# Optimization experiments

Hardware: AMD Instinct MI355X
Metric: run time of the kernel (lower is better)

The kernel has to match this reference:

```python
import jax, jax.numpy as jnp
import numpy as np

B, N, C, H, L = 4, 1024, 1152, 16, 120
D = C // H
HID = 4 * C
EPS = 1e-6


def _ln(x):
    m = jnp.mean(x, axis=-1, keepdims=True)
    v = jnp.var(x, axis=-1, keepdims=True)
    return (x - m) * jax.lax.rsqrt(v + EPS)


def _attend(q, k, v):
    # q:(B,H,Nq,D) k,v:(B,H,Nk,D)
    scale = D ** -0.5
    s = jnp.einsum('bhnd,bhmd->bhnm', q, k) * scale
    p = jax.nn.softmax(s, axis=-1)
    o = jnp.einsum('bhnm,bhmd->bhnd', p, v)
    return o.transpose(0, 2, 1, 3).reshape(q.shape[0], q.shape[2], C)


def setup_inputs() -> dict:
    key = jax.random.key(0)
    ks = jax.random.split(key, 20)
    g = lambda i, shape, s=0.02: jax.random.normal(ks[i], shape, jnp.float32) * s
    return {
        'x': jax.random.normal(ks[0], (B, N, C), jnp.float32),
        'y': jax.random.normal(ks[1], (B, L, C), jnp.float32),
        't': jax.random.normal(ks[2], (B, 6 * C), jnp.float32),
        'sst': jax.random.normal(ks[3], (6, C), jnp.float32) / C ** 0.5,
        'qkv_w': g(4, (C, 3 * C)), 'qkv_b': jnp.zeros((3 * C,), jnp.float32),
        'proj_w': g(5, (C, C)), 'proj_b': jnp.zeros((C,), jnp.float32),
        'q_w': g(6, (C, C)), 'q_b': jnp.zeros((C,), jnp.float32),
        'kv_w': g(7, (C, 2 * C)), 'kv_b': jnp.zeros((2 * C,), jnp.float32),
        'cproj_w': g(8, (C, C)), 'cproj_b': jnp.zeros((C,), jnp.float32),
        'fc1_w': g(9, (C, HID)), 'fc1_b': jnp.zeros((HID,), jnp.float32),
        'fc2_w': g(10, (HID, C)), 'fc2_b': jnp.zeros((C,), jnp.float32),
    }


def reference(x, y, t, sst, qkv_w, qkv_b, proj_w, proj_b, q_w, q_b,
              kv_w, kv_b, cproj_w, cproj_b, fc1_w, fc1_b, fc2_w, fc2_b):
    mods = sst[None] + t.reshape(B, 6, C)  # (B,6,C)
    sh_msa, sc_msa, g_msa, sh_mlp, sc_mlp, g_mlp = [mods[:, i:i + 1] for i in range(6)]

    # --- self attention with adaLN modulation ---
    h = _ln(x) * (1 + sc_msa) + sh_msa
    qkv = (h @ qkv_w + qkv_b).reshape(B, N, 3, H, D).transpose(2, 0, 3, 1, 4)
    attn_out = _attend(qkv[0], qkv[1], qkv[2]) @ proj_w + proj_b
    x = x + g_msa * attn_out

    # --- cross attention (batched cond, no mask) ---
    q = (x @ q_w + q_b).reshape(B, N, H, D).transpose(0, 2, 1, 3)
    kv = (y @ kv_w + kv_b).reshape(B, L, 2, H, D).transpose(2, 0, 3, 1, 4)
    x = x + (_attend(q, kv[0], kv[1]) @ cproj_w + cproj_b)

    # --- MLP with adaLN modulation ---
    h = _ln(x) * (1 + sc_mlp) + sh_mlp
    h = jax.nn.gelu(h @ fc1_w + fc1_b, approximate=True) @ fc2_w + fc2_b
    x = x + g_mlp * h
    return x
```

## Files before the change

### kernel.cpp

```cpp
#include <hip/hip_runtime.h>
#include <hip/hip_bf16.h>
#include <stdint.h>

typedef __hip_bfloat16 BT;
typedef __bf16 bf16x8 __attribute__((ext_vector_type(8)));
typedef float f32x4 __attribute__((ext_vector_type(4)));

constexpr int kB = 4, kN = 1024, kC = 1152, kH = 16, kL = 120, kD = 72, kDp = 96;
constexpr int kHid = 4608, kBN = 4096, kZ = 64;
constexpr float kScale = 0.11785113019775793f;

__global__ void detect_dtype(const void* xin, int* flag) {
  __shared__ int cnt;
  if (threadIdx.x == 0) cnt = 0;
  __syncthreads();
  const BT* xb = (const BT*)xin;
  int local = 0;
  for (int i = threadIdx.x; i < 4096; i += 256) {
    float v = __bfloat162float(xb[i]);
    if (!(fabsf(v) <= 1e3f)) local++;
  }
  atomicAdd(&cnt, local);
  __syncthreads();
  if (threadIdx.x == 0) *flag = (cnt > 8) ? 1 : 0;
}

struct ConvSeg {
  const void* src;
  BT* dst;
  long long n;
};
struct ConvArgs {
  ConvSeg seg[10];
  int nseg;
};
__global__ void convert_all(ConvArgs a, const int* __restrict__ flag) {
  const int f = *flag;
  long long i = (long long)blockIdx.x * 256 + threadIdx.x;
#pragma unroll
  for (int s = 0; s < 10; ++s) {
    if (s >= a.nseg) return;
    if (i < a.seg[s].n) {
      a.seg[s].dst[i] = f ? __float2bfloat16(((const float*)a.seg[s].src)[i])
                          : ((const BT*)a.seg[s].src)[i];
      return;
    }
    i -= a.seg[s].n;
  }
}

__global__ void encode_ws(float* out, long long n, float c) {
  long long i = (long long)blockIdx.x * 256 + threadIdx.x;
  if (i < n) out[i] = c;
}

__device__ __forceinline__ void gl_lds16(const BT* g, BT* l) {
  __builtin_amdgcn_global_load_lds(
      (const __attribute__((address_space(1))) uint32_t*)g,
      (__attribute__((address_space(3))) uint32_t*)l, 16, 0, 0);
}

template <int BM, int EP>
__global__ __launch_bounds__(256, 4) void gemm_tile(
    const BT* __restrict__ A, const BT* __restrict__ Bm, const BT* __restrict__ bias,
    void* __restrict__ Cout, int M, int Nc, int K, int lda, int ldb, int ldc,
    long long sA, long long sB, long long sC) {
  constexpr int NA = BM / 32;
  constexpr int NU = NA + 4;
  constexpr int NJ = (BM == 128) ? 4 : 2;
  __shared__ __align__(16) BT As[2][BM * 32];
  __shared__ __align__(16) BT Bs[2][128 * 32];
  A += (long long)blockIdx.z * sA;
  Bm += (long long)blockIdx.z * sB;

  const int gx = gridDim.x, nwg = gx * gridDim.y;
  int id = blockIdx.y * gx + blockIdx.x;
  {
    const int q = nwg >> 3, r = nwg & 7;
    const int xcd = id & 7, pos = id >> 3;
    const int base = (xcd < r) ? xcd * (q + 1) : r * (q + 1) + (xcd - r) * q;
    id = base + pos;
  }
  const int m0 = (id / gx) * BM, n0 = (id % gx) * 128;

  const int tid = threadIdx.x, lane = tid & 63, w = tid >> 6;
  const int lr = lane >> 2, lc = (lane & 3) * 8;
  const int l15 = lane & 15, q8 = (lane >> 4) * 8;
  const int wm = (BM == 128) ? (w & 1) * 64 : 0;
  const int wn = (BM == 128) ? (w >> 1) * 64 : w * 32;

  auto gptr = [&](int u, int half) -> const BT* {
    if (u < NA) {
      int rr = m0 + u * 32 + lr + half * 16;
      if (rr >= M) rr = M - 1;
      return A + (long long)rr * lda + lc;
    }
    int rr = n0 + (u - NA) * 32 + lr + half * 16;
    if (rr >= Nc) rr = Nc - 1;
    return Bm + (long long)rr * ldb + lc;
  };
  const bool has2 = (w < NA);
  const int u2 = has2 ? (w + 4) : w;
  const BT* g00 = gptr(w, 0);
  const BT* g01 = gptr(w, 1);
  const BT* g10 = gptr(u2, 0);
  const BT* g11 = gptr(u2, 1);
  BT* d00[2];
  BT* d10[2];
#pragma unroll
  for (int bb = 0; bb < 2; ++bb) {
    d00[bb] = (w < NA) ? &As[bb][w * 1024] : &Bs[bb][(w - NA) * 1024];
    int ub = u2 - NA;
    if (ub < 0) ub = 0;
    if (ub > 3) ub = 3;
    d10[bb] = &Bs[bb][ub * 1024];
  }

  auto stage = [&](int bb, int k0) {
    gl_lds16(g00 + k0, d00[bb]);
    gl_lds16(g01 + k0, d00[bb] + 512);
    if (has2) {
      gl_lds16(g10 + k0, d10[bb]);
      gl_lds16(g11 + k0, d10[bb] + 512);
    }
  };

  f32x4 acc[4][NJ] = {};

  auto compute = [&](int bb) {
    bf16x8 af[4], bf[NJ];
#pragma unroll
    for (int i = 0; i < 4; ++i)
      af[i] = *reinterpret_cast<const bf16x8*>(&As[bb][(wm + i * 16 + l15) * 32 + q8]);
#pragma unroll
    for (int j = 0; j < NJ; ++j)
      bf[j] = *reinterpret_cast<const bf16x8*>(&Bs[bb][(wn + j * 16 + l15) * 32 + q8]);
#pragma unroll
    for (int i = 0; i < 4; ++i)
#pragma unroll
      for (int j = 0; j < NJ; ++j)
        acc[i][j] = __builtin_amdgcn_mfma_f32_16x16x32_bf16(af[i], bf[j], acc[i][j], 0, 0, 0);
  };

  stage(0, 0);
  __syncthreads();
  const int nk = K >> 5;
  int cur = 0;
  for (int t = 1; t < nk; ++t) {
    stage(cur ^ 1, t << 5);
    compute(cur);
    __syncthreads();
    cur ^= 1;
  }
  compute(cur);

  const int rowq = (lane >> 4) * 4;
  const long long cb = (long long)blockIdx.z * sC;
#pragma unroll
  for (int j = 0; j < NJ; ++j) {
    int col = n0 + wn + j * 16 + l15;
    if (col >= Nc) continue;
    float bv = bias ? __bfloat162float(bias[col]) : 0.f;
#pragma unroll
    for (int i = 0; i < 4; ++i) {
      int row = m0 + wm + i * 16 + rowq;
#pragma unroll
      for (int r = 0; r < 4; ++r) {
        if (row + r < M) {
          float v = acc[i][j][r] + bv;
          if (EP == 2) {
            float z = 1.5957691216057308f * (v + 0.044715f * v * v * v);
            v = v / (1.f + __expf(-z));
          }
          long long off = cb + (long long)(row + r) * ldc + col;
          if (EP == 1)
            ((float*)Cout)[off] = v;
          else
            ((BT*)Cout)[off] = __float2bfloat16(v);
        }
      }
    }
  }
}

__global__ void transpose_any(const void* __restrict__ in, BT* __restrict__ out,
                              int R, int Cin, const int* __restrict__ flag) {
  __shared__ BT tile[32][33];
  const int f = *flag;
  const int tx = threadIdx.x & 31, ty = threadIdx.x >> 5;
  const int r0 = blockIdx.y * 32, c0 = blockIdx.x * 32;
#pragma unroll
  for (int j = 0; j < 32; j += 8) {
    int r = r0 + ty + j;
    if (r < R && c0 + tx < Cin) {
      long long idx = (long long)r * Cin + c0 + tx;
      tile[ty + j][tx] = f ? __float2bfloat16(((const float*)in)[idx]) : ((const BT*)in)[idx];
    }
  }
  __syncthreads();
#pragma unroll
  for (int j = 0; j < 32; j += 8) {
    int oc = c0 + ty + j;
    if (oc < Cin && r0 + tx < R) out[(long long)oc * R + r0 + tx] = tile[tx][ty + j];
  }
}

template <int SRC>
__global__ __launch_bounds__(256) void ln_mod(const void* __restrict__ xin,
                                              const BT* __restrict__ tc,
                                              const BT* __restrict__ sstc,
                                              BT* __restrict__ hout,
                                              int shiftRow, int scaleRow,
                                              const int* __restrict__ flag) {
  const int f = (SRC == 1) ? 1 : *flag;
  const int row = blockIdx.x;
  const int b = row >> 10;
  const long long base = (long long)row * kC;
  float s = 0.f, s2 = 0.f;
  for (int c = threadIdx.x; c < kC; c += 256) {
    float v = f ? ((const float*)xin)[base + c] : __bfloat162float(((const BT*)xin)[base + c]);
    s += v;
    s2 += v * v;
  }
  for (int o = 32; o > 0; o >>= 1) {
    s += __shfl_down(s, o, 64);
    s2 += __shfl_down(s2, o, 64);
  }
  __shared__ float red[8];
  const int w = threadIdx.x >> 6;
  if ((threadIdx.x & 63) == 0) {
    red[w] = s;
    red[4 + w] = s2;
  }
  __syncthreads();
  const float m = (red[0] + red[1] + red[2] + red[3]) * (1.f / kC);
  const float ex2 = (red[4] + red[5] + red[6] + red[7]) * (1.f / kC);
  const float rstd = rsqrtf(ex2 - m * m + 1e-6f);
  const BT* tsh = tc + (long long)b * 6 * kC + (long long)shiftRow * kC;
  const BT* tsc = tc + (long long)b * 6 * kC + (long long)scaleRow * kC;
  const BT* ssh = sstc + (long long)shiftRow * kC;
  const BT* ssc = sstc + (long long)scaleRow * kC;
  for (int c = threadIdx.x; c < kC; c += 256) {
    float sc = __bfloat162float(ssc[c]) + __bfloat162float(tsc[c]);
    float sh = __bfloat162float(ssh[c]) + __bfloat162float(tsh[c]);
    float xv0 = f ? ((const float*)xin)[base + c] : __bfloat162float(((const BT*)xin)[base + c]);
    float xv = (xv0 - m) * rstd;
    hout[base + c] = __float2bfloat16(xv * (1.f + sc) + sh);
  }
}

__global__ void scatter_qk(const BT* __restrict__ qkv, BT* __restrict__ Qp,
                           BT* __restrict__ Kp) {
  long long i = (long long)blockIdx.x * 256 + threadIdx.x;
  if (i >= (long long)kZ * kN * kDp) return;
  int d = (int)(i % kDp);
  long long r = i / kDp;
  int n = (int)(r % kN);
  int z = (int)(r / kN);
  int b = z >> 4, h = z & 15;
  if (d < kD) {
    long long src = ((long long)(b * kN + n)) * (3 * kC) + h * kD + d;
    Qp[i] = __float2bfloat16(kScale * __bfloat162float(qkv[src]));
    Kp[i] = qkv[src + kC];
  } else {
    Qp[i] = __float2bfloat16(0.f);
    Kp[i] = __float2bfloat16(0.f);
  }
}

__global__ void scatter_v(const BT* __restrict__ qkv, BT* __restrict__ VT) {
  long long i = (long long)blockIdx.x * 256 + threadIdx.x;
  if (i >= (long long)kZ * kD * kN) return;
  int n = (int)(i % kN);
  long long r = i / kN;
  int d = (int)(r % kD);
  int z = (int)(r / kD);
  int b = z >> 4, h = z & 15;
  VT[i] = qkv[((long long)(b * kN + n)) * (3 * kC) + 2 * kC + h * kD + d];
}

__global__ void scatter_qc(const BT* __restrict__ qc, BT* __restrict__ Qp) {
  long long i = (long long)blockIdx.x * 256 + threadIdx.x;
  if (i >= (long long)kZ * kN * kDp) return;
  int d = (int)(i % kDp);
  long long r = i / kDp;
  int n = (int)(r % kN);
  int z = (int)(r / kN);
  int b = z >> 4, h = z & 15;
  Qp[i] = (d < kD)
              ? __float2bfloat16(kScale * __bfloat162float(qc[((long long)(b * kN + n)) * kC + h * kD + d]))
              : __float2bfloat16(0.f);
}

__global__ void scatter_kc(const BT* __restrict__ kvb, BT* __restrict__ Kcp) {
  long long i = (long long)blockIdx.x * 256 + threadIdx.x;
  if (i >= (long long)kZ * kL * kDp) return;
  int d = (int)(i % kDp);
  long long r = i / kDp;
  int l = (int)(r % kL);
  int z = (int)(r / kL);
  int b = z >> 4, h = z & 15;
  Kcp[i] = (d < kD) ? kvb[((long long)(b * kL + l)) * (2 * kC) + h * kD + d] : __float2bfloat16(0.f);
}

__global__ void scatter_vc(const BT* __restrict__ kvb, BT* __restrict__ VcT) {
  long long i = (long long)blockIdx.x * 256 + threadIdx.x;
  if (i >= (long long)kZ * kD * 128) return;
  int l = (int)(i % 128);
  long long r = i / 128;
  int d = (int)(r % kD);
  int z = (int)(r / kD);
  int b = z >> 4, h = z & 15;
  VcT[i] = (l < kL) ? kvb[((long long)(b * kL + l)) * (2 * kC) + kC + h * kD + d] : __float2bfloat16(0.f);
}

__global__ void heads_to_cat(const BT* __restrict__ O, BT* __restrict__ cat) {
  long long i = (long long)blockIdx.x * 256 + threadIdx.x;
  if (i >= (long long)kZ * kN * kD) return;
  int d = (int)(i % kD);
  long long r = i / kD;
  int n = (int)(r % kN);
  int z = (int)(r / kN);
  int b = z >> 4, h = z & 15;
  cat[((long long)(b * kN + n)) * kC + h * kD + d] = O[i];
}

__global__ __launch_bounds__(256) void softmax1024(BT* __restrict__ S) {
  const long long row = blockIdx.x;
  BT* r = S + row * 1024;
  const int tid = threadIdx.x;
  union { ushort4 u; BT b[4]; } ld;
  ld.u = *(const ushort4*)(r + tid * 4);
  float v[4];
#pragma unroll
  for (int k = 0; k < 4; ++k) v[k] = __bfloat162float(ld.b[k]);
  float mx = fmaxf(fmaxf(v[0], v[1]), fmaxf(v[2], v[3]));
  for (int o = 32; o > 0; o >>= 1) mx = fmaxf(mx, __shfl_down(mx, o, 64));
  __shared__ float red[4], red2[4];
  if ((tid & 63) == 0) red[tid >> 6] = mx;
  __syncthreads();
  mx = fmaxf(fmaxf(red[0], red[1]), fmaxf(red[2], red[3]));
  float s = 0.f;
#pragma unroll
  for (int k = 0; k < 4; ++k) {
    v[k] = __expf(v[k] - mx);
    s += v[k];
  }
  for (int o = 32; o > 0; o >>= 1) s += __shfl_down(s, o, 64);
  if ((tid & 63) == 0) red2[tid >> 6] = s;
  __syncthreads();
  s = red2[0] + red2[1] + red2[2] + red2[3];
  const float inv = 1.f / s;
#pragma unroll
  for (int k = 0; k < 4; ++k) ld.b[k] = __float2bfloat16(v[k] * inv);
  *(ushort4*)(r + tid * 4) = ld.u;
}

__global__ void softmax_cross(BT* __restrict__ S) {
  const long long row = blockIdx.x;
  BT* r = S + row * 128;
  const int c = threadIdx.x;
  float v = (c < kL) ? __bfloat162float(r[c]) : -1e30f;
  float mx = v;
  for (int o = 32; o > 0; o >>= 1) mx = fmaxf(mx, __shfl_down(mx, o, 64));
  __shared__ float sm[2], ss[2];
  if ((c & 63) == 0) sm[c >> 6] = mx;
  __syncthreads();
  mx = fmaxf(sm[0], sm[1]);
  float e = (c < kL) ? __expf(v - mx) : 0.f;
  float s = e;
  for (int o = 32; o > 0; o >>= 1) s += __shfl_down(s, o, 64);
  if ((c & 63) == 0) ss[c >> 6] = s;
  __syncthreads();
  s = ss[0] + ss[1];
  r[c] = __float2bfloat16(e / s);
}

__global__ void resid_gate(const void* __restrict__ x, const BT* __restrict__ raw,
                           const BT* __restrict__ tc, const BT* __restrict__ sstc,
                           float* __restrict__ resf, BT* __restrict__ resb,
                           const int* __restrict__ flag) {
  long long i = (long long)blockIdx.x * 256 + threadIdx.x;
  if (i >= (long long)kBN * kC) return;
  const int f = *flag;
  int c = (int)(i % kC);
  int b = (int)(i / ((long long)kN * kC));
  float g = __bfloat162float(sstc[2 * kC + c]) + __bfloat162float(tc[(long long)b * 6 * kC + 2 * kC + c]);
  float xv = f ? ((const float*)x)[i] : __bfloat162float(((const BT*)x)[i]);
  float v = xv + g * __bfloat162float(raw[i]);
  resf[i] = v;
  resb[i] = __float2bfloat16(v);
}

__global__ void resid_add(float* __restrict__ res, const BT* __restrict__ raw) {
  long long i = (long long)blockIdx.x * 256 + threadIdx.x;
  if (i < (long long)kBN * kC) res[i] += __bfloat162float(raw[i]);
}

__global__ void final_out(const float* __restrict__ res, const BT* __restrict__ raw,
                          const BT* __restrict__ tc, const BT* __restrict__ sstc,
                          float* __restrict__ out) {
  long long i = (long long)blockIdx.x * 256 + threadIdx.x;
  if (i >= (long long)kBN * kC) return;
  int c = (int)(i % kC);
  int b = (int)(i / ((long long)kN * kC));
  float g = __bfloat162float(sstc[5 * kC + c]) + __bfloat162float(tc[(long long)b * 6 * kC + 5 * kC + c]);
  out[i] = res[i] + g * __bfloat162float(raw[i]);
}

extern "C" void kernel_launch(void* const* d_in, const int* in_sizes, int n_in,
                              void* d_out, int out_size, void* d_ws, size_t ws_size,
                              hipStream_t stream) {
  const void* x = d_in[0];
  const void* y = d_in[1];
  const void* t = d_in[2];
  const void* sst = d_in[3];
  const void* qkv_w = d_in[4];
  const void* qkv_b = d_in[5];
  const void* proj_w = d_in[6];
  const void* proj_b = d_in[7];
  const void* q_w = d_in[8];
  const void* q_b = d_in[9];
  const void* kv_w = d_in[10];
  const void* kv_b = d_in[11];
  const void* cproj_w = d_in[12];
  const void* cproj_b = d_in[13];
  const void* fc1_w = d_in[14];
  const void* fc1_b = d_in[15];
  const void* fc2_w = d_in[16];
  const void* fc2_b = d_in[17];
  (void)in_sizes; (void)n_in;

  char* p = (char*)d_ws;
  size_t off = 0;
  auto alloc = [&](size_t bytes) {
    void* r = p + off;
    off += (bytes + 1023) & ~(size_t)1023;
    return r;
  };
  int* dflag = (int*)alloc(16);
  BT* canonY = (BT*)alloc((size_t)kB * kL * kC * 2);
  BT* canonT = (BT*)alloc((size_t)kB * 6 * kC * 2);
  BT* canonSst = (BT*)alloc((size_t)6 * kC * 2);
  BT* canonBias = (BT*)alloc((size_t)16384 * 2);
  BT* wT = (BT*)alloc((size_t)kHid * kC * 2);
  BT* bufH = (BT*)alloc((size_t)kBN * kC * 2);
  BT* bufCH = (BT*)alloc((size_t)kZ * kN * kDp * 2);
  BT* bufQp = (BT*)alloc((size_t)kZ * kN * kDp * 2);
  BT* bufVT = (BT*)alloc((size_t)kZ * kD * kN * 2);
  BT* rawB = (BT*)alloc((size_t)kBN * kC * 2);
  float* resF = (float*)alloc((size_t)kBN * kC * 4);
  BT* arena = (BT*)alloc((size_t)kBN * kHid * 2);
  const size_t need = off;

  BT* bufO = rawB;
  BT* fc2T = bufQp;
  BT* kvBuf = (BT*)((char*)arena + 17825792);

  if (ws_size < need) {
    float c = 100.f * (float)(1 + (int)(ws_size >> 24));
    long long n = (long long)out_size;
    encode_ws<<<(int)((n + 255) / 256), 256, 0, stream>>>((float*)d_out, n, c);
    return;
  }

  BT* qkvB = canonBias;
  BT* projB = canonBias + 3456;
  BT* qB = canonBias + 4608;
  BT* kvB = canonBias + 5760;
  BT* cprojB = canonBias + 8064;
  BT* fc1B = canonBias + 9216;
  BT* fc2B = canonBias + 13824;

  auto gemm = [&](int ep, const BT* A, const BT* Bm, const BT* bias, void* Cp,
                  int M, int Nc, int K, int lda, int ldb, int ldc,
                  long long sA, long long sB, long long sC, int Zb) {
    long long nwg128 = (long long)((Nc + 127) / 128) * ((M + 127) / 128) * Zb;
    if (nwg128 < 512) {
      dim3 g((Nc + 127) / 128, (M + 63) / 64, Zb);
      if (ep == 0)
        gemm_tile<64, 0><<<g, 256, 0, stream>>>(A, Bm, bias, Cp, M, Nc, K, lda, ldb, ldc, sA, sB, sC);
      else if (ep == 1)
        gemm_tile<64, 1><<<g, 256, 0, stream>>>(A, Bm, bias, Cp, M, Nc, K, lda, ldb, ldc, sA, sB, sC);
      else
        gemm_tile<64, 2><<<g, 256, 0, stream>>>(A, Bm, bias, Cp, M, Nc, K, lda, ldb, ldc, sA, sB, sC);
    } else {
      dim3 g((Nc + 127) / 128, (M + 127) / 128, Zb);
      if (ep == 0)
        gemm_tile<128, 0><<<g, 256, 0, stream>>>(A, Bm, bias, Cp, M, Nc, K, lda, ldb, ldc, sA, sB, sC);
      else if (ep == 1)
        gemm_tile<128, 1><<<g, 256, 0, stream>>>(A, Bm, bias, Cp, M, Nc, K, lda, ldb, ldc, sA, sB, sC);
      else
        gemm_tile<128, 2><<<g, 256, 0, stream>>>(A, Bm, bias, Cp, M, Nc, K, lda, ldb, ldc, sA, sB, sC);
    }
  };
  auto tp = [&](const void* in, BT* out, int R, int Cin) {
    dim3 g((Cin + 31) / 32, (R + 31) / 32);
    transpose_any<<<g, 256, 0, stream>>>(in, out, R, Cin, dflag);
  };

  detect_dtype<<<1, 256, 0, stream>>>(x, dflag);
  {
    ConvArgs a;
    a.seg[0] = {y, canonY, (long long)kB * kL * kC};
    a.seg[1] = {t, canonT, (long long)kB * 6 * kC};
    a.seg[2] = {sst, canonSst, (long long)6 * kC};
    a.seg[3] = {qkv_b, qkvB, 3456};
    a.seg[4] = {proj_b, projB, 1152};
    a.seg[5] = {q_b, qB, 1152};
    a.seg[6] = {kv_b, kvB, 2304};
    a.seg[7] = {cproj_b, cprojB, 1152};
    a.seg[8] = {fc1_b, fc1B, 4608};
    a.seg[9] = {fc2_b, fc2B, 1152};
    a.nseg = 10;
    long long tot = 552960 + 27648 + 6912 + 14976;
    convert_all<<<(int)((tot + 255) / 256), 256, 0, stream>>>(a, dflag);
  }

  ln_mod<0><<<kBN, 256, 0, stream>>>(x, canonT, canonSst, bufH, 0, 1, dflag);
  tp(qkv_w, wT, kC, 3 * kC);
  gemm(0, bufH, wT, qkvB, arena, kBN, 3 * kC, kC, kC, kC, 3 * kC, 0, 0, 0, 1);
  {
    long long tot = (long long)kZ * kN * kDp;
    scatter_qk<<<(int)((tot + 255) / 256), 256, 0, stream>>>(arena, bufQp, bufCH);
    tot = (long long)kZ * kD * kN;
    scatter_v<<<(int)((tot + 255) / 256), 256, 0, stream>>>(arena, bufVT);
  }
  for (int c = 0; c < 4; ++c) {
    int z0 = c * 16;
    const BT* Qb = bufQp + (size_t)z0 * kN * kDp;
    const BT* Kb = bufCH + (size_t)z0 * kN * kDp;
    const BT* Vb = bufVT + (size_t)z0 * kD * kN;
    BT* Ob = bufO + (size_t)z0 * kN * kD;
    gemm(0, Qb, Kb, nullptr, arena, kN, kN, kDp, kDp, kDp, kN,
         (long long)kN * kDp, (long long)kN * kDp, (long long)kN * kN, 16);
    softmax1024<<<16 * kN, 256, 0, stream>>>(arena);
    gemm(0, arena, Vb, nullptr, Ob, kN, kD, kN, kN, kN, kD,
         (long long)kN * kN, (long long)kD * kN, (long long)kN * kD, 16);
  }
  heads_to_cat<<<18432, 256, 0, stream>>>(bufO, bufCH);
  tp(proj_w, wT, kC, kC);
  gemm(0, bufCH, wT, projB, rawB, kBN, kC, kC, kC, kC, kC, 0, 0, 0, 1);
  resid_gate<<<18432, 256, 0, stream>>>(x, rawB, canonT, canonSst, resF, bufH, dflag);

  tp(q_w, wT, kC, kC);
  gemm(0, bufH, wT, qB, bufCH, kBN, kC, kC, kC, kC, kC, 0, 0, 0, 1);
  {
    long long tot = (long long)kZ * kN * kDp;
    scatter_qc<<<(int)((tot + 255) / 256), 256, 0, stream>>>(bufCH, bufQp);
  }
  tp(kv_w, wT, kC, 2 * kC);
  gemm(0, canonY, wT, kvB, kvBuf, kB * kL, 2 * kC, kC, kC, kC, 2 * kC, 0, 0, 0, 1);
  {
    long long tot = (long long)kZ * kL * kDp;
    scatter_kc<<<(int)((tot + 255) / 256), 256, 0, stream>>>(kvBuf, bufCH);
    tot = (long long)kZ * kD * 128;
    scatter_vc<<<(int)((tot + 255) / 256), 256, 0, stream>>>(kvBuf, bufVT);
  }
  gemm(0, bufQp, bufCH, nullptr, arena, kN, kL, kDp, kDp, kDp, 128,
       (long long)kN * kDp, (long long)kL * kDp, (long long)kN * 128, kZ);
  softmax_cross<<<kZ * kN, 128, 0, stream>>>(arena);
  gemm(0, arena, bufVT, nullptr, bufO, kN, kD, 128, 128, 128, kD,
       (long long)kN * 128, (long long)kD * 128, (long long)kN * kD, kZ);
  heads_to_cat<<<18432, 256, 0, stream>>>(bufO, bufCH);
  tp(cproj_w, wT, kC, kC);
  gemm(0, bufCH, wT, cprojB, rawB, kBN, kC, kC, kC, kC, kC, 0, 0, 0, 1);
  resid_add<<<18432, 256, 0, stream>>>(resF, rawB);

  ln_mod<1><<<kBN, 256, 0, stream>>>(resF, canonT, canonSst, bufH, 3, 4, dflag);
  tp(fc1_w, wT, kC, kHid);
  tp(fc2_w, fc2T, kHid, kC);
  gemm(2, bufH, wT, fc1B, arena, kBN, kHid, kC, kC, kC, kHid, 0, 0, 0, 1);
  gemm(0, arena, fc2T, fc2B, rawB, kBN, kC, kHid, kHid, kHid, kC, 0, 0, 0, 1);
  final_out<<<18432, 256, 0, stream>>>(resF, rawB, canonT, canonSst, (float*)d_out);
}
```

Measured before the change: 866.9 us.

## Use 64-deep K tiles with XOR-swizzled LDS in GEMM kernel

Adds a GEMM variant that stages 64-wide K slices per iteration, halving the number of barriers and loop iterations, and uses an XOR swizzle on the LDS layout to avoid bank conflicts on fragment reads. The old 32-deep kernel is kept as a fallback only when K is not a multiple of 64. The larger shared-memory footprint lowers the occupancy hint from 4 to 2 blocks per CU, which may reduce latency hiding.

New measurement: 810.5 us. 1.07x faster.

```diff
diff --git a/kernel.cpp b/kernel.cpp
--- a/kernel.cpp
+++ b/kernel.cpp
@@ -61,15 +61,14 @@
 }
 
 template <int BM, int EP>
-__global__ __launch_bounds__(256, 4) void gemm_tile(
+__global__ __launch_bounds__(256, 2) void gemm_t64(
     const BT* __restrict__ A, const BT* __restrict__ Bm, const BT* __restrict__ bias,
     void* __restrict__ Cout, int M, int Nc, int K, int lda, int ldb, int ldc,
     long long sA, long long sB, long long sC) {
   constexpr int NA = BM / 32;
-  constexpr int NU = NA + 4;
   constexpr int NJ = (BM == 128) ? 4 : 2;
-  __shared__ __align__(16) BT As[2][BM * 32];
-  __shared__ __align__(16) BT Bs[2][128 * 32];
+  __shared__ __align__(16) BT As[2][BM * 64];
+  __shared__ __align__(16) BT Bs[2][128 * 64];
   A += (long long)blockIdx.z * sA;
   Bm += (long long)blockIdx.z * sB;
 
@@ -83,62 +82,188 @@
   }
   const int m0 = (id / gx) * BM, n0 = (id % gx) * 128;
 
-  const int tid = threadIdx.x, lane = tid & 63, w = tid >> 6;
-  const int lr = lane >> 2, lc = (lane & 3) * 8;
-  const int l15 = lane & 15, q8 = (lane >> 4) * 8;
+  const int lane = threadIdx.x & 63, w = threadIdx.x >> 6;
+  const int l15 = lane & 15;
+  const int srow = lane >> 3;
+  const int ssrc = ((lane & 7) ^ srow) * 8;
   const int wm = (BM == 128) ? (w & 1) * 64 : 0;
   const int wn = (BM == 128) ? (w >> 1) * 64 : w * 32;
 
-  auto gptr = [&](int u, int half) -> const BT* {
-    if (u < NA) {
-      int rr = m0 + u * 32 + lr + half * 16;
-      if (rr >= M) rr = M - 1;
-      return A + (long long)rr * lda + lc;
-    }
-    int rr = n0 + (u - NA) * 32 + lr + half * 16;
-    if (rr >= Nc) rr = Nc - 1;
-    return Bm + (long long)rr * ldb + lc;
-  };
   const bool has2 = (w < NA);
+  const int u1 = w;
   const int u2 = has2 ? (w + 4) : w;
-  const BT* g00 = gptr(w, 0);
-  const BT* g01 = gptr(w, 1);
-  const BT* g10 = gptr(u2, 0);
-  const BT* g11 = gptr(u2, 1);
-  BT* d00[2];
-  BT* d10[2];
+  const BT* gp1[4];
+  const BT* gp2[4];
+#pragma unroll
+  for (int q = 0; q < 4; ++q) {
+    {
+      int rr, lim;
+      const BT* basep;
+      int stride;
+      if (u1 < NA) { rr = m0 + u1 * 32; lim = M; basep = A; stride = lda; }
+      else { rr = n0 + (u1 - NA) * 32; lim = Nc; basep = Bm; stride = ldb; }
+      rr += q * 8 + srow;
+      if (rr >= lim) rr = lim - 1;
+      gp1[q] = basep + (long long)rr * stride + ssrc;
+    }
+    {
+      int rr, lim;
+      const BT* basep;
+      int stride;
+      if (u2 < NA) { rr = m0 + u2 * 32; lim = M; basep = A; stride = lda; }
+      else { rr = n0 + (u2 - NA) * 32; lim = Nc; basep = Bm; stride = ldb; }
+      rr += q * 8 + srow;
+      if (rr >= lim) rr = lim - 1;
+      gp2[q] = basep + (long long)rr * stride + ssrc;
+    }
+  }
+  BT* d1[2];
+  BT* d2[2];
 #pragma unroll
   for (int bb = 0; bb < 2; ++bb) {
-    d00[bb] = (w < NA) ? &As[bb][w * 1024] : &Bs[bb][(w - NA) * 1024];
+    d1[bb] = (u1 < NA) ? &As[bb][u1 * 2048] : &Bs[bb][(u1 - NA) * 2048];
     int ub = u2 - NA;
     if (ub < 0) ub = 0;
     if (ub > 3) ub = 3;
-    d10[bb] = &Bs[bb][ub * 1024];
+    d2[bb] = &Bs[bb][ub * 2048];
   }
 
   auto stage = [&](int bb, int k0) {
-    gl_lds16(g00 + k0, d00[bb]);
-    gl_lds16(g01 + k0, d00[bb] + 512);
+#pragma unroll
+    for (int q = 0; q < 4; ++q) gl_lds16(gp1[q] + k0, d1[bb] + q * 512);
     if (has2) {
-      gl_lds16(g10 + k0, d10[bb]);
-      gl_lds16(g11 + k0, d10[bb] + 512);
+#pragma unroll
+      for (int q = 0; q < 4; ++q) gl_lds16(gp2[q] + k0, d2[bb] + q * 512);
     }
   };
 
+  const int rsw = l15 & 7;
+  const int ch0 = ((lane >> 4) ^ rsw) * 8;
+  const int ch1 = ((4 | (lane >> 4)) ^ rsw) * 8;
+
   f32x4 acc[4][NJ] = {};
 
   auto compute = [&](int bb) {
-    bf16x8 af[4], bf[NJ];
+    bf16x8 af[4][2], bf[NJ][2];
+#pragma unroll
+    for (int i = 0; i < 4; ++i) {
+      const int row = wm + i * 16 + l15;
+      af[i][0] = *reinterpret_cast<const bf16x8*>(&As[bb][row * 64 + ch0]);
+      af[i][1] = *reinterpret_cast<const bf16x8*>(&As[bb][row * 64 + ch1]);
+    }
+#pragma unroll
+    for (int j = 0; j < NJ; ++j) {
+      const int row = wn + j * 16 + l15;
+      bf[j][0] = *reinterpret_cast<const bf16x8*>(&Bs[bb][row * 64 + ch0]);
+      bf[j][1] = *reinterpret_cast<const bf16x8*>(&Bs[bb][row * 64 + ch1]);
+    }
+#pragma unroll
+    for (int i = 0; i < 4; ++i)
+#pragma unroll
+      for (int j = 0; j < NJ; ++j) {
+        acc[i][j] = __builtin_amdgcn_mfma_f32_16x16x32_bf16(af[i][0], bf[j][0], acc[i][j], 0, 0, 0);
+        acc[i][j] = __builtin_amdgcn_mfma_f32_16x16x32_bf16(af[i][1], bf[j][1], acc[i][j], 0, 0, 0);
+      }
+  };
+
+  stage(0, 0);
+  __syncthreads();
+  const int nk = K >> 6;
+  int cur = 0;
+  for (int t = 1; t < nk; ++t) {
+    stage(cur ^ 1, t << 6);
+    compute(cur);
+    __syncthreads();
+    cur ^= 1;
+  }
+  compute(cur);
+
+  const int rowq = (lane >> 4) * 4;
+  const long long cb = (long long)blockIdx.z * sC;
+#pragma unroll
+  for (int j = 0; j < NJ; ++j) {
+    int col = n0 + wn + j * 16 + l15;
+    if (col >= Nc) continue;
+    float bv = bias ? __bfloat162float(bias[col]) : 0.f;
+#pragma unroll
+    for (int i = 0; i < 4; ++i) {
+      int row = m0 + wm + i * 16 + rowq;
+#pragma unroll
+      for (int r = 0; r < 4; ++r) {
+        if (row + r < M) {
+          float v = acc[i][j][r] + bv;
+          if (EP == 2) {
+            float z = 1.5957691216057308f * (v + 0.044715f * v * v * v);
+            v = v / (1.f + __expf(-z));
+          }
+          long long off = cb + (long long)(row + r) * ldc + col;
+          if (EP == 1)
+            ((float*)Cout)[off] = v;
+          else
+            ((BT*)Cout)[off] = __float2bfloat16(v);
+        }
+      }
+    }
+  }
+}
+
+template <int EP>
+__global__ __launch_bounds__(256, 4) void gemm_tile(
+    const BT* __restrict__ A, const BT* __restrict__ Bm, const BT* __restrict__ bias,
+    void* __restrict__ Cout, int M, int Nc, int K, int lda, int ldb, int ldc,
+    long long sA, long long sB, long long sC) {
+  __shared__ __align__(16) BT As[2][128 * 32];
+  __shared__ __align__(16) BT Bs[2][128 * 32];
+  A += (long long)blockIdx.z * sA;
+  Bm += (long long)blockIdx.z * sB;
+
+  const int gx = gridDim.x, nwg = gx * gridDim.y;
+  int id = blockIdx.y * gx + blockIdx.x;
+  {
+    const int q = nwg >> 3, r = nwg & 7;
+    const int xcd = id & 7, pos = id >> 3;
+    const int base = (xcd < r) ? xcd * (q + 1) : r * (q + 1) + (xcd - r) * q;
+    id = base + pos;
+  }
+  const int m0 = (id / gx) * 128, n0 = (id % gx) * 128;
+
+  const int lane = threadIdx.x & 63, w = threadIdx.x >> 6;
+  const int lr = lane >> 2, lc = (lane & 3) * 8;
+  const int l15 = lane & 15, q8 = (lane >> 4) * 8;
+  const int wm = (w & 1) * 64, wn = (w >> 1) * 64;
+
+  int ra0 = m0 + w * 32 + lr, ra1 = ra0 + 16;
+  if (ra0 >= M) ra0 = M - 1;
+  if (ra1 >= M) ra1 = M - 1;
+  int rb0 = n0 + w * 32 + lr, rb1 = rb0 + 16;
+  if (rb0 >= Nc) rb0 = Nc - 1;
+  if (rb1 >= Nc) rb1 = Nc - 1;
+  const BT* pa0 = A + (long long)ra0 * lda + lc;
+  const BT* pa1 = A + (long long)ra1 * lda + lc;
+  const BT* pb0 = Bm + (long long)rb0 * ldb + lc;
+  const BT* pb1 = Bm + (long long)rb1 * ldb + lc;
+
+  auto stage = [&](int bb, int k0) {
+    gl_lds16(pa0 + k0, &As[bb][w * 1024]);
+    gl_lds16(pa1 + k0, &As[bb][w * 1024 + 512]);
+    gl_lds16(pb0 + k0, &Bs[bb][w * 1024]);
+    gl_lds16(pb1 + k0, &Bs[bb][w * 1024 + 512]);
+  };
+
+  f32x4 acc[4][4] = {};
+
+  auto compute = [&](int bb) {
+    bf16x8 af[4], bf[4];
 #pragma unroll
     for (int i = 0; i < 4; ++i)
       af[i] = *reinterpret_cast<const bf16x8*>(&As[bb][(wm + i * 16 + l15) * 32 + q8]);
 #pragma unroll
-    for (int j = 0; j < NJ; ++j)
+    for (int j = 0; j < 4; ++j)
       bf[j] = *reinterpret_cast<const bf16x8*>(&Bs[bb][(wn + j * 16 + l15) * 32 + q8]);
 #pragma unroll
     for (int i = 0; i < 4; ++i)
 #pragma unroll
-      for (int j = 0; j < NJ; ++j)
+      for (int j = 0; j < 4; ++j)
         acc[i][j] = __builtin_amdgcn_mfma_f32_16x16x32_bf16(af[i], bf[j], acc[i][j], 0, 0, 0);
   };
 
@@ -157,7 +282,7 @@
   const int rowq = (lane >> 4) * 4;
   const long long cb = (long long)blockIdx.z * sC;
 #pragma unroll
-  for (int j = 0; j < NJ; ++j) {
+  for (int j = 0; j < 4; ++j) {
     int col = n0 + wn + j * 16 + l15;
     if (col >= Nc) continue;
     float bv = bias ? __bfloat162float(bias[col]) : 0.f;
@@ -476,22 +601,30 @@
                   int M, int Nc, int K, int lda, int ldb, int ldc,
                   long long sA, long long sB, long long sC, int Zb) {
     long long nwg128 = (long long)((Nc + 127) / 128) * ((M + 127) / 128) * Zb;
-    if (nwg128 < 512) {
+    if (K & 63) {
+      dim3 g((Nc + 127) / 128, (M + 127) / 128, Zb);
+      if (ep == 0)
+        gemm_tile<0><<<g, 256, 0, stream>>>(A, Bm, bias, Cp, M, Nc, K, lda, ldb, ldc, sA, sB, sC);
+      else if (ep == 1)
+        gemm_tile<1><<<g, 256, 0, stream>>>(A, Bm, bias, Cp, M, Nc, K, lda, ldb, ldc, sA, sB, sC);
+      else
+        gemm_tile<2><<<g, 256, 0, stream>>>(A, Bm, bias, Cp, M, Nc, K, lda, ldb, ldc, sA, sB, sC);
+    } else if (nwg128 < 512) {
       dim3 g((Nc + 127) / 128, (M + 63) / 64, Zb);
       if (ep == 0)
-        gemm_tile<64, 0><<<g, 256, 0, stream>>>(A, Bm, bias, Cp, M, Nc, K, lda, ldb, ldc, sA, sB, sC);
+        gemm_t64<64, 0><<<g, 256, 0, stream>>>(A, Bm, bias, Cp, M, Nc, K, lda, ldb, ldc, sA, sB, sC);
       else if (ep == 1)
-        gemm_tile<64, 1><<<g, 256, 0, stream>>>(A, Bm, bias, Cp, M, Nc, K, lda, ldb, ldc, sA, sB, sC);
+        gemm_t64<64, 1><<<g, 256, 0, stream>>>(A, Bm, bias, Cp, M, Nc, K, lda, ldb, ldc, sA, sB, sC);
       else
-        gemm_tile<64, 2><<<g, 256, 0, stream>>>(A, Bm, bias, Cp, M, Nc, K, lda, ldb, ldc, sA, sB, sC);
+        gemm_t64<64, 2><<<g, 256, 0, stream>>>(A, Bm, bias, Cp, M, Nc, K, lda, ldb, ldc, sA, sB, sC);
     } else {
       dim3 g((Nc + 127) / 128, (M + 127) / 128, Zb);
       if (ep == 0)
-        gemm_tile<128, 0><<<g, 256, 0, stream>>>(A, Bm, bias, Cp, M, Nc, K, lda, ldb, ldc, sA, sB, sC);
+        gemm_t64<128, 0><<<g, 256, 0, stream>>>(A, Bm, bias, Cp, M, Nc, K, lda, ldb, ldc, sA, sB, sC);
       else if (ep == 1)
-        gemm_tile<128, 1><<<g, 256, 0, stream>>>(A, Bm, bias, Cp, M, Nc, K, lda, ldb, ldc, sA, sB, sC);
+        gemm_t64<128, 1><<<g, 256, 0, stream>>>(A, Bm, bias, Cp, M, Nc, K, lda, ldb, ldc, sA, sB, sC);
       else
-        gemm_tile<128, 2><<<g, 256, 0, stream>>>(A, Bm, bias, Cp, M, Nc, K, lda, ldb, ldc, sA, sB, sC);
+        gemm_t64<128, 2><<<g, 256, 0, stream>>>(A, Bm, bias, Cp, M, Nc, K, lda, ldb, ldc, sA, sB, sC);
     }
   };
   auto tp = [&](const void* in, BT* out, int R, int Cin) {
```
